# Performance work log

Hardware: AMD Instinct MI355X
Metric: run time of the kernel (lower is better)

Reference implementation:

```python
import jax, jax.numpy as jnp
import numpy as np

IN_CHANNELS = 64
OUT_CHANNELS = 64
SEQ_LEN = 512
KERNEL_SIZE = 9
STRIDE = 1
PADDING = 4  # symmetric
OUT_SEQ_LEN = (SEQ_LEN + 2 * PADDING - (KERNEL_SIZE - 1) - 1) // STRIDE + 1  # 512


def setup_inputs() -> dict:
    key = jax.random.key(0)
    k1, k2, k3 = jax.random.split(key, 3)
    x = jax.random.normal(k1, (64, IN_CHANNELS, SEQ_LEN), dtype=jnp.float32)
    # nn.init.normal_(std=0.1)
    weight = 0.1 * jax.random.normal(k2, (IN_CHANNELS, OUT_CHANNELS, KERNEL_SIZE, OUT_SEQ_LEN), dtype=jnp.float32)
    bias = 0.1 * jax.random.normal(k3, (OUT_CHANNELS, OUT_SEQ_LEN), dtype=jnp.float32)
    return {"x": x, "weight": weight, "bias": bias}


def reference(x, weight, bias):
    # x: [B, Ci, S] -> pad last dim
    xp = jnp.pad(x, ((0, 0), (0, 0), (PADDING, PADDING)))
    # Unfold (im2col) as a gather: same math as the one-hot grouped conv.
    starts = jnp.arange(OUT_SEQ_LEN) * STRIDE            # [L]
    offs = jnp.arange(KERNEL_SIZE)                        # [K]
    idx = starts[:, None] + offs[None, :]                 # [L, K]
    patches = xp[:, :, idx]                               # [B, Ci, L, K]
    # per-position matmul: 'b i l k, i o k l -> b o l'
    out = jnp.einsum('bilk,iokl->bol', patches, weight)
    out = out + bias                                      # [B, Co, L]
    return out
```

## Files before the change

kernel.cpp:

```cpp
#include <hip/hip_runtime.h>


#define CIN   64
#define COUT  64
#define SEQ   512
#define KS    9
#define LT    16
#define OT    8
#define LWIN  24
#define WSTR  (COUT*KS*SEQ)
#define XBS   40
#define XLW   (64*XBS)
#define XS_ELEMS (LWIN*XLW)
#define BOS   40
#define BLS   (OT*BOS + 8)
#define BSLOT (LT*BLS)
#define ZOFF  (XS_ELEMS + 2*BSLOT)
#define LDS_USH (ZOFF + 64)
#define LDS_BYTES (LDS_USH*2)
#define NSTEP 18

typedef __attribute__((ext_vector_type(8))) short bf16x8;
typedef __attribute__((ext_vector_type(4))) float f32x4;

__device__ __forceinline__ uint pack2bf(float a0, float a1) {
    uint u0 = __float_as_uint(a0) + 0x8000u;
    uint u1 = __float_as_uint(a1) + 0x8000u;
    return __builtin_amdgcn_perm(u1, u0, 0x07060302);
}

__global__ __launch_bounds__(1024, 4)
void lc1d_mfma(const float* __restrict__ x, const float* __restrict__ w,
               const float* __restrict__ bias, float* __restrict__ out)
{
    extern __shared__ ushort lds[];
    ushort* Xs = lds;
    ushort* BsB = lds + XS_ELEMS;

    const int tid  = threadIdx.x;
    const int lane = tid & 63;
    const int wvid = tid >> 6;
    const int bt = wvid & 3;
    const int lg = wvid >> 2;
    const int lt = blockIdx.x >> 3;
    const int os = blockIdx.x & 7;
    const int l0 = lt * LT;
    const int o0 = os * OT;

    const bool stager = (tid < 512);
    const int lf  = tid & 3;
    const int oo  = (tid >> 2) & 7;
    const int ipp = (tid >> 5) & 15;

    const float* wbase = w + ((size_t)(2*ipp)*COUT + (o0 + oo))*(KS*SEQ) + l0 + lf*4;

    float4 rA[3], rB[3];

    #define LOAD_RING(sl, s) if (stager && (s) < NSTEP) {                        \
        const int ih_ = (s) / 9, k_ = (s) - 9*ih_;                               \
        const float* p_ = wbase + (size_t)ih_*32*WSTR + k_*SEQ;                  \
        rA[sl] = *(const float4*)p_;                                             \
        rB[sl] = *(const float4*)(p_ + WSTR);                                    \
    }

    #define WRITE_BS(sl, s) if (stager) {                                        \
        ushort* dst_ = BsB + ((s)&1)*BSLOT + oo*BOS + 2*ipp;                     \
        _Pragma("unroll")                                                        \
        for (int dl = 0; dl < 4; ++dl) {                                         \
            uint pk_ = pack2bf((&rA[sl].x)[dl], (&rB[sl].x)[dl]);                \
            *(uint*)(dst_ + (lf*4+dl)*BLS) = pk_;                                \
        }                                                                        \
    }

    #define STAGE_XS(ih) {                                                       \
        const int qq  = tid & 7;                                                 \
        const int rp0 = tid >> 3;                                                \
        if (qq < 6) {                                                            \
            _Pragma("unroll")                                                    \
            for (int it = 0; it < 8; ++it) {                                     \
                const int rp = rp0 + it*128;                                     \
                const int b_ = rp >> 4, ip_ = rp & 15;                           \
                const float* s0 = x + ((size_t)(b_*CIN) + (ih)*32 + 2*ip_)*SEQ   \
                                    + (l0 - 4) + qq*4;                           \
                float4 v0 = make_float4(0.f,0.f,0.f,0.f), v1 = v0;               \
                if (!((lt == 0 && qq == 0) || (lt == 31 && qq == 5))) {          \
                    v0 = *(const float4*)s0;                                     \
                    v1 = *(const float4*)(s0 + SEQ);                             \
                }                                                                \
                ushort* d_ = Xs + b_*XBS + 2*ip_;                                \
                _Pragma("unroll")                                                \
                for (int dl = 0; dl < 4; ++dl)                                   \
                    *(uint*)(d_ + (qq*4+dl)*XLW) = pack2bf((&v0.x)[dl],          \
                                                           (&v1.x)[dl]);         \
            }                                                                    \
        }                                                                        \
    }

    const int aoff = (bt*16 + (lane & 15))*XBS + (lane >> 4)*8;
    const int boff = (lane & 15)*BOS + (lane >> 4)*8;
    const bool nhi = (lane & 15) >= 8;
    const ushort* zptr = lds + ZOFF + (lane >> 4)*8;

    f32x4 acc[4];
    #pragma unroll
    for (int j = 0; j < 4; ++j) acc[j] = (f32x4)0.0f;

    #define DO_MFMA(s) {                                                         \
        const int k_ = (s) % 9;                                                  \
        const ushort* BsS = BsB + ((s)&1)*BSLOT;                                 \
        _Pragma("unroll")                                                        \
        for (int dl = 0; dl < 4; ++dl) {                                         \
            const int ll = lg*4 + dl;                                            \
            bf16x8 Af = *(const bf16x8*)(Xs + (ll + k_)*XLW + aoff);             \
            const ushort* Bp = nhi ? zptr : (BsS + ll*BLS + boff);               \
            bf16x8 Bf = *(const bf16x8*)Bp;                                      \
            acc[dl] = __builtin_amdgcn_mfma_f32_16x16x32_bf16(Af, Bf, acc[dl],   \
                                                              0, 0, 0);          \
        }                                                                        \
    }

    #define STEP(s) {                                                            \
        if ((s) < NSTEP-1) WRITE_BS(((s)+1)%3, (s)+1)                            \
        LOAD_RING(((s)+1)%3, (s)+4)                                              \
        DO_MFMA(s)                                                               \
        __syncthreads();                                                         \
    }

    LOAD_RING(0, 0)
    LOAD_RING(1, 1)
    LOAD_RING(2, 2)
    if (tid < 64) lds[ZOFF + tid] = 0;
    STAGE_XS(0)
    WRITE_BS(0, 0)
    LOAD_RING(0, 3)
    __syncthreads();

    STEP(0)  STEP(1)  STEP(2)  STEP(3)  STEP(4)
    STEP(5)  STEP(6)  STEP(7)  STEP(8)

    STAGE_XS(1)
    __syncthreads();

    STEP(9)  STEP(10) STEP(11) STEP(12) STEP(13)
    STEP(14) STEP(15) STEP(16) STEP(17)

    if (!nhi) {
        const int og = o0 + (lane & 15);
        const int rb = (lane >> 4)*4;
        #pragma unroll
        for (int dl = 0; dl < 4; ++dl) {
            const int lgl = l0 + lg*4 + dl;
            const float bv = bias[og*SEQ + lgl];
            #pragma unroll
            for (int r = 0; r < 4; ++r) {
                const int bg = bt*16 + rb + r;
                out[((size_t)(bg*COUT + og))*SEQ + lgl] = acc[dl][r] + bv;
            }
        }
    }
}

extern "C" void kernel_launch(void* const* d_in, const int* in_sizes, int n_in,
                              void* d_out, int out_size, void* d_ws, size_t ws_size,
                              hipStream_t stream) {
    const float* x    = (const float*)d_in[0];
    const float* wgt  = (const float*)d_in[1];
    const float* bias = (const float*)d_in[2];
    float* out        = (float*)d_out;

    hipFuncSetAttribute((const void*)lc1d_mfma,
                        hipFuncAttributeMaxDynamicSharedMemorySize, LDS_BYTES);
    dim3 grid(256);
    lc1d_mfma<<<grid, 1024, LDS_BYTES, stream>>>(x, wgt, bias, out);
}
```

Before: 134.1 us.

## Specialize warps into producer stagers and MFMA consumers with swizzled X LDS

Splits the 16 waves into 8 weight-staging waves and 8 compute waves. Each compute wave now handles two batch tiles, so it reuses each B fragment across two MFMAs. The X tile in LDS is XOR-swizzled on write and read to reduce bank conflicts on A-fragment loads. This overlaps global weight loads with MFMA work, but halves the number of waves issuing MFMAs and doubles accumulator registers per compute wave.

```diff
diff --git a/kernel.cpp b/kernel.cpp
--- a/kernel.cpp
+++ b/kernel.cpp
@@ -40,14 +40,12 @@
     const int tid  = threadIdx.x;
     const int lane = tid & 63;
     const int wvid = tid >> 6;
-    const int bt = wvid & 3;
-    const int lg = wvid >> 2;
     const int lt = blockIdx.x >> 3;
     const int os = blockIdx.x & 7;
     const int l0 = lt * LT;
     const int o0 = os * OT;
 
-    const bool stager = (tid < 512);
+    const bool stager = (wvid < 8);
     const int lf  = tid & 3;
     const int oo  = (tid >> 2) & 7;
     const int ipp = (tid >> 5) & 15;
@@ -76,6 +74,7 @@
         const int qq  = tid & 7;                                                 \
         const int rp0 = tid >> 3;                                                \
         if (qq < 6) {                                                            \
+            const int sw = 8*(qq & 3);                                           \
             _Pragma("unroll")                                                    \
             for (int it = 0; it < 8; ++it) {                                     \
                 const int rp = rp0 + it*128;                                     \
@@ -87,7 +86,7 @@
                     v0 = *(const float4*)s0;                                     \
                     v1 = *(const float4*)(s0 + SEQ);                             \
                 }                                                                \
-                ushort* d_ = Xs + b_*XBS + 2*ip_;                                \
+                ushort* d_ = Xs + b_*XBS + ((2*ip_) ^ sw);                       \
                 _Pragma("unroll")                                                \
                 for (int dl = 0; dl < 4; ++dl)                                   \
                     *(uint*)(d_ + (qq*4+dl)*XLW) = pack2bf((&v0.x)[dl],          \
@@ -96,26 +95,38 @@
         }                                                                        \
     }
 
-    const int aoff = (bt*16 + (lane & 15))*XBS + (lane >> 4)*8;
+    const int cw  = wvid - 8;
+    const int lg  = cw & 3;
+    const int bth = cw >> 2;
+    const int am  = (lane & 15) * XBS;
+    const int akg = (lane >> 4) * 8;
     const int boff = (lane & 15)*BOS + (lane >> 4)*8;
     const bool nhi = (lane & 15) >= 8;
     const ushort* zptr = lds + ZOFF + (lane >> 4)*8;
 
-    f32x4 acc[4];
+    f32x4 acc[2][4];
     #pragma unroll
-    for (int j = 0; j < 4; ++j) acc[j] = (f32x4)0.0f;
+    for (int a = 0; a < 2; ++a)
+        #pragma unroll
+        for (int j = 0; j < 4; ++j) acc[a][j] = (f32x4)0.0f;
 
-    #define DO_MFMA(s) {                                                         \
+    #define DO_MFMA(s) if (!stager) {                                            \
         const int k_ = (s) % 9;                                                  \
         const ushort* BsS = BsB + ((s)&1)*BSLOT;                                 \
         _Pragma("unroll")                                                        \
         for (int dl = 0; dl < 4; ++dl) {                                         \
             const int ll = lg*4 + dl;                                            \
-            bf16x8 Af = *(const bf16x8*)(Xs + (ll + k_)*XLW + aoff);             \
+            const int lw = ll + k_;                                              \
+            const int rot = ((lw >> 2) & 3) * 8;                                 \
             const ushort* Bp = nhi ? zptr : (BsS + ll*BLS + boff);               \
             bf16x8 Bf = *(const bf16x8*)Bp;                                      \
-            acc[dl] = __builtin_amdgcn_mfma_f32_16x16x32_bf16(Af, Bf, acc[dl],   \
-                                                              0, 0, 0);          \
+            const ushort* Ar = Xs + lw*XLW + am + (akg ^ rot);                   \
+            _Pragma("unroll")                                                    \
+            for (int b2 = 0; b2 < 2; ++b2) {                                     \
+                bf16x8 Af = *(const bf16x8*)(Ar + (bth*2 + b2)*(16*XBS));        \
+                acc[b2][dl] = __builtin_amdgcn_mfma_f32_16x16x32_bf16(           \
+                                  Af, Bf, acc[b2][dl], 0, 0, 0);                 \
+            }                                                                    \
         }                                                                        \
     }
 
@@ -144,7 +155,7 @@
     STEP(9)  STEP(10) STEP(11) STEP(12) STEP(13)
     STEP(14) STEP(15) STEP(16) STEP(17)
 
-    if (!nhi) {
+    if (!stager && !nhi) {
         const int og = o0 + (lane & 15);
         const int rb = (lane >> 4)*4;
         #pragma unroll
@@ -152,9 +163,12 @@
             const int lgl = l0 + lg*4 + dl;
             const float bv = bias[og*SEQ + lgl];
             #pragma unroll
-            for (int r = 0; r < 4; ++r) {
-                const int bg = bt*16 + rb + r;
-                out[((size_t)(bg*COUT + og))*SEQ + lgl] = acc[dl][r] + bv;
+            for (int b2 = 0; b2 < 2; ++b2) {
+                #pragma unroll
+                for (int r = 0; r < 4; ++r) {
+                    const int bg = (bth*2 + b2)*16 + rb + r;
+                    out[((size_t)(bg*COUT + og))*SEQ + lgl] = acc[b2][dl][r] + bv;
+                }
             }
         }
     }
```

Result: no change. 134.5 us (+0.4%).
